# Performance work log

Hardware: AMD Instinct MI355X
Metric: run time of the kernel (lower is better)

Reference implementation:

```python
import jax, jax.numpy as jnp
import numpy as np


def _phi(z, conv_w, conv_b):
    # z: (H, W, S, 1) -> 3x3 SAME conv over state channels -> softmax over states
    x = jnp.transpose(z[..., 0], (2, 0, 1))[None]  # (1, S, H, W)
    y = jax.lax.conv_general_dilated(
        x, conv_w, window_strides=(1, 1), padding='SAME',
        dimension_numbers=('NCHW', 'OIHW', 'NCHW')) + conv_b[None, :, None, None]
    return jax.nn.softmax(jnp.transpose(y[0], (1, 2, 0)), axis=2)[..., None]  # (H, W, S, 1)


def _update(obs, P, u_k, w_k_O, conv_w, conv_b):
    H, W, O = obs.shape
    S = P.shape[0]
    # b = P^T @ obs per cell: b[h,w,s] = sum_o P[o,s] * obs[h,w,o]
    b = jnp.einsum('os,hwo->hws', P, obs)[..., None]  # (H, W, S, 1)
    # Analytic Jacobian db/dP: deriv_b[h,w,s,0,i,j] = obs[h,w,i] * delta(s==j)
    eye = jnp.eye(S, O, dtype=obs.dtype)
    deriv_b = (obs[:, :, None, :, None] * eye[None, None, :, None, :])[:, :, :, None, :, :]  # (H,W,S,1,S,O)

    Bu = b * u_k                                  # (H, W, S, 1)
    bu = jnp.sum(Bu, axis=2, keepdims=True)       # (H, W, 1, 1)
    Z = Bu / bu                                   # Bu / bu

    u_kp1 = _phi(Z, conv_w, conv_b)               # (H, W, S, 1)

    # Sensitivity recursion for obs params (quotient rule on Bu/bu)
    du = deriv_b * u_k[..., None, None] + b[..., None, None] * w_k_O  # (H,W,S,1,S,O)
    term1 = du * bu[..., None, None]
    term2 = jnp.expand_dims(jnp.sum(du, axis=2), 3) * Bu[..., None, None]
    w_pre = (term1 - term2) / bu[..., None, None] ** 2                # (H,W,S,1,S,O)

    # J @ w  ==  9 JVPs of Phi at Z with tangent columns of w (exact, avoids dense (HWS)^2 Jacobian)
    tangents = jnp.moveaxis(w_pre.reshape(H, W, S, 1, S * O), -1, 0)  # (S*O, H, W, S, 1)
    jvp1 = lambda t: jax.jvp(lambda z: _phi(z, conv_w, conv_b), (Z,), (t,))[1]
    w_kp1_O = jnp.moveaxis(jax.vmap(jvp1)(tangents), 0, -1).reshape(H, W, S, 1, S, O)
    return u_kp1, w_kp1_O


def setup_inputs() -> dict:
    key = jax.random.key(0)
    k1, k2, k3 = jax.random.split(key, 3)
    H = W = 512
    S = O = 3
    obs = jax.random.uniform(k1, (H, W, O), dtype=jnp.float32)
    obs_param_matrix = jnp.ones((S, O), jnp.float32) / O          # row-stochastic init
    u_k = jnp.ones((H, W, S, 1), jnp.float32) / S                 # uniform belief
    w_k_O = jnp.zeros((H, W, S, 1, S, O), jnp.float32)
    conv_w = jax.random.normal(k2, (S, S, 3, 3), jnp.float32) * 0.1
    conv_b = jax.random.normal(k3, (S,), jnp.float32) * 0.1
    return {'obs': obs, 'obs_param_matrix': obs_param_matrix, 'u_k': u_k,
            'w_k_O': w_k_O, 'conv_w': conv_w, 'conv_b': conv_b}


def reference(obs, obs_param_matrix, u_k, w_k_O, conv_w, conv_b):
    return _update(obs, obs_param_matrix, u_k, w_k_O, conv_w, conv_b)
```

## Files before the change

kernel.cpp:

```cpp
#include <hip/hip_runtime.h>

#define IMH 512
#define IMW 512
#define TW 16
#define TH 16
#define HW_ (TW + 2)
#define HH_ (TH + 2)
#define NHALO (HW_ * HH_)
#define ROW 31

__global__ __launch_bounds__(256, 4)
void hmm_fused(const float* __restrict__ obs,
               const float* __restrict__ P,
               const float* __restrict__ u_k,
               const float* __restrict__ w_k,
               const float* __restrict__ conv_w,
               const float* __restrict__ conv_b,
               float* __restrict__ out) {
    __shared__ float lds[NHALO * ROW];

    const int tid = threadIdx.x;
    const int w0 = blockIdx.x * TW;
    const int h0 = blockIdx.y * TH;

    float Pm[9];
#pragma unroll
    for (int i = 0; i < 9; ++i) Pm[i] = P[i];

    for (int p = tid; p < NHALO; p += 256) {
        const int hh = h0 + p / HW_ - 1;
        const int ww = w0 + p % HW_ - 1;
        float* row = &lds[p * ROW];
        if (hh < 0 || hh >= IMH || ww < 0 || ww >= IMW) {
#pragma unroll
            for (int c = 0; c < 30; ++c) row[c] = 0.0f;
            continue;
        }
        const int pix = hh * IMW + ww;
        const float ov[3] = {obs[pix * 3 + 0], obs[pix * 3 + 1], obs[pix * 3 + 2]};
        const float us[3] = {u_k[pix * 3 + 0], u_k[pix * 3 + 1], u_k[pix * 3 + 2]};

        float b[3], Bu[3], bu = 0.0f;
#pragma unroll
        for (int s = 0; s < 3; ++s) {
            b[s] = Pm[0 * 3 + s] * ov[0] + Pm[1 * 3 + s] * ov[1] + Pm[2 * 3 + s] * ov[2];
            Bu[s] = b[s] * us[s];
            bu += Bu[s];
        }
        const float inv_bu = 1.0f / bu;
        float Z[3];
#pragma unroll
        for (int s = 0; s < 3; ++s) { Z[s] = Bu[s] * inv_bu; row[s] = Z[s]; }

        const float* wkp = &w_k[(size_t)pix * 27];
#pragma unroll
        for (int i = 0; i < 3; ++i) {
#pragma unroll
            for (int j = 0; j < 3; ++j) {
                const int ij = i * 3 + j;
                float du[3], sdu = 0.0f;
#pragma unroll
                for (int s = 0; s < 3; ++s) {
                    float d = b[s] * wkp[s * 9 + ij];
                    if (s == j) d += ov[i] * us[s];
                    du[s] = d;
                    sdu += d;
                }
#pragma unroll
                for (int s = 0; s < 3; ++s)
                    row[(1 + ij) * 3 + s] = (du[s] - sdu * Z[s]) * inv_bu;
            }
        }
    }

    float cw[81];
#pragma unroll
    for (int i = 0; i < 81; ++i) cw[i] = conv_w[i];
    const float cb[3] = {conv_b[0], conv_b[1], conv_b[2]};

    __syncthreads();

    const int tx = tid % TW, ty = tid / TW;
    const int hp = (ty + 1) * HW_ + (tx + 1);
    const int pix = (h0 + ty) * IMW + (w0 + tx);

    float p0, p1, p2;
    {
        float y[3] = {cb[0], cb[1], cb[2]};
#pragma unroll
        for (int ky = 0; ky < 3; ++ky) {
#pragma unroll
            for (int kx = 0; kx < 3; ++kx) {
                const float* nb = &lds[(hp + (ky - 1) * HW_ + (kx - 1)) * ROW];
                const float v0 = nb[0], v1 = nb[1], v2 = nb[2];
#pragma unroll
                for (int s = 0; s < 3; ++s)
                    y[s] += cw[s * 27 + 0 * 9 + ky * 3 + kx] * v0 +
                            cw[s * 27 + 1 * 9 + ky * 3 + kx] * v1 +
                            cw[s * 27 + 2 * 9 + ky * 3 + kx] * v2;
            }
        }
        const float m = fmaxf(y[0], fmaxf(y[1], y[2]));
        const float e0 = __expf(y[0] - m), e1 = __expf(y[1] - m), e2 = __expf(y[2] - m);
        const float inv = 1.0f / (e0 + e1 + e2);
        p0 = e0 * inv; p1 = e1 * inv; p2 = e2 * inv;
        out[pix * 3 + 0] = p0; out[pix * 3 + 1] = p1; out[pix * 3 + 2] = p2;
    }

    float wout[27];
#pragma unroll
    for (int g = 1; g < 10; ++g) {
        float a[3] = {0.0f, 0.0f, 0.0f};
#pragma unroll
        for (int ky = 0; ky < 3; ++ky) {
#pragma unroll
            for (int kx = 0; kx < 3; ++kx) {
                const float* nb = &lds[(hp + (ky - 1) * HW_ + (kx - 1)) * ROW];
                const float v0 = nb[g * 3 + 0], v1 = nb[g * 3 + 1], v2 = nb[g * 3 + 2];
#pragma unroll
                for (int s = 0; s < 3; ++s)
                    a[s] += cw[s * 27 + 0 * 9 + ky * 3 + kx] * v0 +
                            cw[s * 27 + 1 * 9 + ky * 3 + kx] * v1 +
                            cw[s * 27 + 2 * 9 + ky * 3 + kx] * v2;
            }
        }
        const float dot = p0 * a[0] + p1 * a[1] + p2 * a[2];
        const int ij = g - 1;
        wout[0 * 9 + ij] = p0 * (a[0] - dot);
        wout[1 * 9 + ij] = p1 * (a[1] - dot);
        wout[2 * 9 + ij] = p2 * (a[2] - dot);
    }

    __syncthreads();

#pragma unroll
    for (int c = 0; c < 27; ++c) lds[tid * 27 + c] = wout[c];
    __syncthreads();

    float* outw = out + IMH * IMW * 3;
    for (int idx = tid; idx < TW * TH * 27; idx += 256) {
        const int r = idx / (TW * 27);
        const int rem = idx - r * (TW * 27);
        outw[(h0 + r) * (IMW * 27) + w0 * 27 + rem] = lds[idx];
    }
}

extern "C" void kernel_launch(void* const* d_in, const int* in_sizes, int n_in,
                              void* d_out, int out_size, void* d_ws, size_t ws_size,
                              hipStream_t stream) {
    const float* obs    = (const float*)d_in[0];
    const float* P      = (const float*)d_in[1];
    const float* u_k    = (const float*)d_in[2];
    const float* w_k    = (const float*)d_in[3];
    const float* conv_w = (const float*)d_in[4];
    const float* conv_b = (const float*)d_in[5];
    float* out = (float*)d_out;

    dim3 grid(IMW / TW, IMH / TH);
    hmm_fused<<<grid, 256, 0, stream>>>(obs, P, u_k, w_k, conv_w, conv_b, out);
}
```

Baseline: 117.6 us.

## Split tile into two 16x8 halves with register prefetch and row-sliding conv work split

Each block now covers two 16x8 sub-tiles. Global loads for both halos are issued up front with vectorized loads into registers, so the second half's fetch overlaps the first half's compute. The 9 JVP channel groups are spread across threads: one thread per pixel handles the primal softmax plus the last group, and the other groups run in a row-sliding register pipeline with direct global stores, replacing the LDS staging write-back. This trades higher register pressure and scattered 27-strided stores for better latency hiding and work distribution.

```diff
diff --git a/kernel.cpp b/kernel.cpp
--- a/kernel.cpp
+++ b/kernel.cpp
@@ -3,11 +3,164 @@
 #define IMH 512
 #define IMW 512
 #define TW 16
-#define TH 16
+#define TH 8
 #define HW_ (TW + 2)
 #define HH_ (TH + 2)
 #define NHALO (HW_ * HH_)
+#define NPIX (TW * TH)
 #define ROW 31
+
+typedef float f4 __attribute__((ext_vector_type(4)));
+typedef float f4a __attribute__((ext_vector_type(4), aligned(4)));
+typedef float f2a __attribute__((ext_vector_type(2), aligned(4)));
+
+
+#define LOADPX(HH, WW, WREG, OV, US, OK) {                                        \
+    (OK) = !((HH) < 0 || (HH) >= IMH || (WW) < 0 || (WW) >= IMW);                 \
+    if (OK) {                                                                     \
+        const int pix_ = (HH) * IMW + (WW);                                       \
+        const f2a o01_ = *(const f2a*)(obs + pix_ * 3);                           \
+        (OV)[0] = o01_.x; (OV)[1] = o01_.y; (OV)[2] = obs[pix_ * 3 + 2];          \
+        const f2a u01_ = *(const f2a*)(u_k + pix_ * 3);                           \
+        (US)[0] = u01_.x; (US)[1] = u01_.y; (US)[2] = u_k[pix_ * 3 + 2];          \
+        const float* wkp_ = &w_k[(size_t)pix_ * 27];                              \
+        const f4a* v4_ = (const f4a*)wkp_;                                        \
+        const f4a a0_ = v4_[0], a1_ = v4_[1], a2_ = v4_[2];                       \
+        const f4a a3_ = v4_[3], a4_ = v4_[4], a5_ = v4_[5];                       \
+        const f2a a6_ = *(const f2a*)(wkp_ + 24);                                 \
+        (WREG)[0]=a0_.x;  (WREG)[1]=a0_.y;  (WREG)[2]=a0_.z;  (WREG)[3]=a0_.w;    \
+        (WREG)[4]=a1_.x;  (WREG)[5]=a1_.y;  (WREG)[6]=a1_.z;  (WREG)[7]=a1_.w;    \
+        (WREG)[8]=a2_.x;  (WREG)[9]=a2_.y;  (WREG)[10]=a2_.z; (WREG)[11]=a2_.w;   \
+        (WREG)[12]=a3_.x; (WREG)[13]=a3_.y; (WREG)[14]=a3_.z; (WREG)[15]=a3_.w;   \
+        (WREG)[16]=a4_.x; (WREG)[17]=a4_.y; (WREG)[18]=a4_.z; (WREG)[19]=a4_.w;   \
+        (WREG)[20]=a5_.x; (WREG)[21]=a5_.y; (WREG)[22]=a5_.z; (WREG)[23]=a5_.w;   \
+        (WREG)[24]=a6_.x; (WREG)[25]=a6_.y; (WREG)[26]=wkp_[26];                  \
+    } }
+
+#define TRANSFORM(OK, WREG, OV, US, PIDX) {                                       \
+    float* row_ = &lds[(PIDX) * ROW];                                             \
+    if (!(OK)) {                                                                  \
+        _Pragma("unroll") for (int c = 0; c < 30; ++c) row_[c] = 0.0f;            \
+    } else {                                                                      \
+        float b_[3], Bu_[3], bu_ = 0.0f;                                          \
+        _Pragma("unroll")                                                         \
+        for (int s = 0; s < 3; ++s) {                                             \
+            b_[s] = Pm[0 + s] * (OV)[0] + Pm[3 + s] * (OV)[1] + Pm[6 + s] * (OV)[2]; \
+            Bu_[s] = b_[s] * (US)[s];                                             \
+            bu_ += Bu_[s];                                                        \
+        }                                                                         \
+        const float inv_bu_ = 1.0f / bu_;                                         \
+        float Z_[3];                                                              \
+        _Pragma("unroll")                                                         \
+        for (int s = 0; s < 3; ++s) { Z_[s] = Bu_[s] * inv_bu_; row_[s] = Z_[s]; }\
+        _Pragma("unroll")                                                         \
+        for (int i = 0; i < 3; ++i) {                                             \
+            _Pragma("unroll")                                                     \
+            for (int j = 0; j < 3; ++j) {                                         \
+                const int ij_ = i * 3 + j;                                        \
+                float du_[3], sdu_ = 0.0f;                                        \
+                _Pragma("unroll")                                                 \
+                for (int s = 0; s < 3; ++s) {                                     \
+                    float d_ = b_[s] * (WREG)[s * 9 + ij_];                       \
+                    if (s == j) d_ += (OV)[i] * (US)[s];                          \
+                    du_[s] = d_;                                                  \
+                    sdu_ += d_;                                                   \
+                }                                                                 \
+                _Pragma("unroll")                                                 \
+                for (int s = 0; s < 3; ++s)                                       \
+                    row_[(1 + ij_) * 3 + s] = (du_[s] - sdu_ * Z_[s]) * inv_bu_;  \
+            }                                                                     \
+        }                                                                         \
+    } }
+
+#define B0_BODY(H0T)                                                              \
+    if (tid < NPIX) {                                                             \
+        const int tx = tid & 15, ty = tid >> 4;                                   \
+        const int hp = (ty + 1) * HW_ + (tx + 1);                                 \
+        const int pix = ((H0T) + ty) * IMW + (w0 + tx);                           \
+        float y0 = cb0, y1 = cb1, y2 = cb2;                                       \
+        _Pragma("unroll")                                                         \
+        for (int ky = 0; ky < 3; ++ky) {                                          \
+            _Pragma("unroll")                                                     \
+            for (int kx = 0; kx < 3; ++kx) {                                      \
+                const float* nb = &lds[(hp + (ky - 1) * HW_ + (kx - 1)) * ROW];   \
+                const float v0 = nb[0], v1 = nb[1], v2 = nb[2];                   \
+                const int T = ky * 3 + kx;                                        \
+                y0 += cw[0 + T] * v0 + cw[9 + T] * v1 + cw[18 + T] * v2;          \
+                y1 += cw[27 + T] * v0 + cw[36 + T] * v1 + cw[45 + T] * v2;        \
+                y2 += cw[54 + T] * v0 + cw[63 + T] * v1 + cw[72 + T] * v2;        \
+            }                                                                     \
+        }                                                                         \
+        const float m_ = fmaxf(y0, fmaxf(y1, y2));                                \
+        const float e0 = __expf(y0 - m_), e1 = __expf(y1 - m_), e2 = __expf(y2 - m_); \
+        const float inv_ = 1.0f / (e0 + e1 + e2);                                 \
+        const float p0 = e0 * inv_, p1 = e1 * inv_, p2 = e2 * inv_;               \
+        out[pix * 3 + 0] = p0; out[pix * 3 + 1] = p1; out[pix * 3 + 2] = p2;      \
+        p_aux4[tid] = (f4){p0, p1, p2, 0.0f};                                     \
+        float a0 = 0.0f, a1 = 0.0f, a2 = 0.0f;                                    \
+        _Pragma("unroll")                                                         \
+        for (int ky = 0; ky < 3; ++ky) {                                          \
+            _Pragma("unroll")                                                     \
+            for (int kx = 0; kx < 3; ++kx) {                                      \
+                const float* nb = &lds[(hp + (ky - 1) * HW_ + (kx - 1)) * ROW];   \
+                const float v0 = nb[27], v1 = nb[28], v2 = nb[29];                \
+                const int T = ky * 3 + kx;                                        \
+                a0 += cw[0 + T] * v0 + cw[9 + T] * v1 + cw[18 + T] * v2;          \
+                a1 += cw[27 + T] * v0 + cw[36 + T] * v1 + cw[45 + T] * v2;        \
+                a2 += cw[54 + T] * v0 + cw[63 + T] * v1 + cw[72 + T] * v2;        \
+            }                                                                     \
+        }                                                                         \
+        const float dot_ = p0 * a0 + p1 * a1 + p2 * a2;                           \
+        float* wp = outw + (size_t)pix * 27;                                      \
+        wp[8]  = p0 * (a0 - dot_);                                                \
+        wp[17] = p1 * (a1 - dot_);                                                \
+        wp[26] = p2 * (a2 - dot_);                                                \
+    }
+
+#define ROWFMA(P0_, P1_, P2_, KY)                                                 \
+    P0_ += cw[0 + (KY)*3 + 0] * v00 + cw[9 + (KY)*3 + 0] * v01 + cw[18 + (KY)*3 + 0] * v02; \
+    P1_ += cw[27 + (KY)*3 + 0] * v00 + cw[36 + (KY)*3 + 0] * v01 + cw[45 + (KY)*3 + 0] * v02; \
+    P2_ += cw[54 + (KY)*3 + 0] * v00 + cw[63 + (KY)*3 + 0] * v01 + cw[72 + (KY)*3 + 0] * v02; \
+    P0_ += cw[0 + (KY)*3 + 1] * v10 + cw[9 + (KY)*3 + 1] * v11 + cw[18 + (KY)*3 + 1] * v12; \
+    P1_ += cw[27 + (KY)*3 + 1] * v10 + cw[36 + (KY)*3 + 1] * v11 + cw[45 + (KY)*3 + 1] * v12; \
+    P2_ += cw[54 + (KY)*3 + 1] * v10 + cw[63 + (KY)*3 + 1] * v11 + cw[72 + (KY)*3 + 1] * v12; \
+    P0_ += cw[0 + (KY)*3 + 2] * v20 + cw[9 + (KY)*3 + 2] * v21 + cw[18 + (KY)*3 + 2] * v22; \
+    P1_ += cw[27 + (KY)*3 + 2] * v20 + cw[36 + (KY)*3 + 2] * v21 + cw[45 + (KY)*3 + 2] * v22; \
+    P2_ += cw[54 + (KY)*3 + 2] * v20 + cw[63 + (KY)*3 + 2] * v21 + cw[72 + (KY)*3 + 2] * v22;
+
+#define FINISH(O, Q0, Q1, Q2) {                                                   \
+    const f4 pv = p_aux4[(O) * 16 + x];                                           \
+    const float dotf_ = pv.x * (Q0) + pv.y * (Q1) + pv.z * (Q2);                  \
+    float* wp_ = outw + ((size_t)((h0t + (O)) * IMW + (w0 + x))) * 27 + ij;       \
+    wp_[0]  = pv.x * ((Q0) - dotf_);                                              \
+    wp_[9]  = pv.y * ((Q1) - dotf_);                                              \
+    wp_[18] = pv.z * ((Q2) - dotf_); }
+
+#define STEP(R, N0,N1,N2, M0,M1,M2, O0,O1,O2, DO_N, DO_M, DO_O) {                 \
+    const int rb = ((rowb + (R)) * HW_ + x) * ROW + gch;                          \
+    const float v00 = lds[rb + 0],  v01 = lds[rb + 1],  v02 = lds[rb + 2];        \
+    const float v10 = lds[rb + 31], v11 = lds[rb + 32], v12 = lds[rb + 33];       \
+    const float v20 = lds[rb + 62], v21 = lds[rb + 63], v22 = lds[rb + 64];       \
+    if (DO_N) { N0 = 0.0f; N1 = 0.0f; N2 = 0.0f; ROWFMA(N0, N1, N2, 0) }          \
+    if (DO_M) { ROWFMA(M0, M1, M2, 1) }                                           \
+    if (DO_O) { ROWFMA(O0, O1, O2, 2) FINISH(rowb + (R) - 2, O0, O1, O2) } }
+
+#define B1_BODY(H0T) {                                                            \
+    const int h0t = (H0T);                                                        \
+    const int x = tid & 15;                                                       \
+    const int g = ((tid >> 4) & 7) + 1;                                           \
+    const int ij = g - 1;                                                         \
+    const int gch = 3 * g;                                                        \
+    const int hlf = tid >> 7;                                                     \
+    const int rowb = hlf * 4;                                                     \
+    float a00, a01, a02, b10, b11, b12, c20, c21, c22;                            \
+    STEP(0, a00,a01,a02, b10,b11,b12, c20,c21,c22, true,  false, false)           \
+    STEP(1, b10,b11,b12, a00,a01,a02, c20,c21,c22, true,  true,  false)           \
+    STEP(2, c20,c21,c22, b10,b11,b12, a00,a01,a02, true,  true,  true )           \
+    STEP(3, a00,a01,a02, c20,c21,c22, b10,b11,b12, true,  true,  true )           \
+    STEP(4, b10,b11,b12, a00,a01,a02, c20,c21,c22, false, true,  true )           \
+    STEP(5, c20,c21,c22, b10,b11,b12, a00,a01,a02, false, false, true )           \
+    }
 
 __global__ __launch_bounds__(256, 4)
 void hmm_fused(const float* __restrict__ obs,
@@ -17,132 +170,48 @@
                const float* __restrict__ conv_w,
                const float* __restrict__ conv_b,
                float* __restrict__ out) {
-    __shared__ float lds[NHALO * ROW];
+    __shared__ __align__(16) float lds[NHALO * ROW];
+    __shared__ f4 p_aux4[NPIX];
 
     const int tid = threadIdx.x;
     const int w0 = blockIdx.x * TW;
-    const int h0 = blockIdx.y * TH;
+    const int h0a = blockIdx.y * (2 * TH);
+    const int h0b = h0a + TH;
 
     float Pm[9];
 #pragma unroll
     for (int i = 0; i < 9; ++i) Pm[i] = P[i];
-
-    for (int p = tid; p < NHALO; p += 256) {
-        const int hh = h0 + p / HW_ - 1;
-        const int ww = w0 + p % HW_ - 1;
-        float* row = &lds[p * ROW];
-        if (hh < 0 || hh >= IMH || ww < 0 || ww >= IMW) {
-#pragma unroll
-            for (int c = 0; c < 30; ++c) row[c] = 0.0f;
-            continue;
-        }
-        const int pix = hh * IMW + ww;
-        const float ov[3] = {obs[pix * 3 + 0], obs[pix * 3 + 1], obs[pix * 3 + 2]};
-        const float us[3] = {u_k[pix * 3 + 0], u_k[pix * 3 + 1], u_k[pix * 3 + 2]};
-
-        float b[3], Bu[3], bu = 0.0f;
-#pragma unroll
-        for (int s = 0; s < 3; ++s) {
-            b[s] = Pm[0 * 3 + s] * ov[0] + Pm[1 * 3 + s] * ov[1] + Pm[2 * 3 + s] * ov[2];
-            Bu[s] = b[s] * us[s];
-            bu += Bu[s];
-        }
-        const float inv_bu = 1.0f / bu;
-        float Z[3];
-#pragma unroll
-        for (int s = 0; s < 3; ++s) { Z[s] = Bu[s] * inv_bu; row[s] = Z[s]; }
-
-        const float* wkp = &w_k[(size_t)pix * 27];
-#pragma unroll
-        for (int i = 0; i < 3; ++i) {
-#pragma unroll
-            for (int j = 0; j < 3; ++j) {
-                const int ij = i * 3 + j;
-                float du[3], sdu = 0.0f;
-#pragma unroll
-                for (int s = 0; s < 3; ++s) {
-                    float d = b[s] * wkp[s * 9 + ij];
-                    if (s == j) d += ov[i] * us[s];
-                    du[s] = d;
-                    sdu += d;
-                }
-#pragma unroll
-                for (int s = 0; s < 3; ++s)
-                    row[(1 + ij) * 3 + s] = (du[s] - sdu * Z[s]) * inv_bu;
-            }
-        }
-    }
-
     float cw[81];
 #pragma unroll
     for (int i = 0; i < 81; ++i) cw[i] = conv_w[i];
-    const float cb[3] = {conv_b[0], conv_b[1], conv_b[2]};
-
-    __syncthreads();
-
-    const int tx = tid % TW, ty = tid / TW;
-    const int hp = (ty + 1) * HW_ + (tx + 1);
-    const int pix = (h0 + ty) * IMW + (w0 + tx);
-
-    float p0, p1, p2;
-    {
-        float y[3] = {cb[0], cb[1], cb[2]};
-#pragma unroll
-        for (int ky = 0; ky < 3; ++ky) {
-#pragma unroll
-            for (int kx = 0; kx < 3; ++kx) {
-                const float* nb = &lds[(hp + (ky - 1) * HW_ + (kx - 1)) * ROW];
-                const float v0 = nb[0], v1 = nb[1], v2 = nb[2];
-#pragma unroll
-                for (int s = 0; s < 3; ++s)
-                    y[s] += cw[s * 27 + 0 * 9 + ky * 3 + kx] * v0 +
-                            cw[s * 27 + 1 * 9 + ky * 3 + kx] * v1 +
-                            cw[s * 27 + 2 * 9 + ky * 3 + kx] * v2;
-            }
-        }
-        const float m = fmaxf(y[0], fmaxf(y[1], y[2]));
-        const float e0 = __expf(y[0] - m), e1 = __expf(y[1] - m), e2 = __expf(y[2] - m);
-        const float inv = 1.0f / (e0 + e1 + e2);
-        p0 = e0 * inv; p1 = e1 * inv; p2 = e2 * inv;
-        out[pix * 3 + 0] = p0; out[pix * 3 + 1] = p1; out[pix * 3 + 2] = p2;
+    const float cb0 = conv_b[0], cb1 = conv_b[1], cb2 = conv_b[2];
+
+    float* outw = out + IMH * IMW * 3;
+
+    float wreg1[27], ov1[3], us1[3];
+    bool ok1 = false;
+
+    if (tid < NHALO) {
+        const int ph = tid / HW_ - 1, pw = tid % HW_ - 1;
+        float wreg0[27], ov0[3], us0[3];
+        bool ok0;
+        LOADPX(h0a + ph, w0 + pw, wreg0, ov0, us0, ok0)
+        LOADPX(h0b + ph, w0 + pw, wreg1, ov1, us1, ok1)
+        TRANSFORM(ok0, wreg0, ov0, us0, tid)
     }
-
-    float wout[27];
-#pragma unroll
-    for (int g = 1; g < 10; ++g) {
-        float a[3] = {0.0f, 0.0f, 0.0f};
-#pragma unroll
-        for (int ky = 0; ky < 3; ++ky) {
-#pragma unroll
-            for (int kx = 0; kx < 3; ++kx) {
-                const float* nb = &lds[(hp + (ky - 1) * HW_ + (kx - 1)) * ROW];
-                const float v0 = nb[g * 3 + 0], v1 = nb[g * 3 + 1], v2 = nb[g * 3 + 2];
-#pragma unroll
-                for (int s = 0; s < 3; ++s)
-                    a[s] += cw[s * 27 + 0 * 9 + ky * 3 + kx] * v0 +
-                            cw[s * 27 + 1 * 9 + ky * 3 + kx] * v1 +
-                            cw[s * 27 + 2 * 9 + ky * 3 + kx] * v2;
-            }
-        }
-        const float dot = p0 * a[0] + p1 * a[1] + p2 * a[2];
-        const int ij = g - 1;
-        wout[0 * 9 + ij] = p0 * (a[0] - dot);
-        wout[1 * 9 + ij] = p1 * (a[1] - dot);
-        wout[2 * 9 + ij] = p2 * (a[2] - dot);
-    }
-
-    __syncthreads();
-
-#pragma unroll
-    for (int c = 0; c < 27; ++c) lds[tid * 27 + c] = wout[c];
-    __syncthreads();
-
-    float* outw = out + IMH * IMW * 3;
-    for (int idx = tid; idx < TW * TH * 27; idx += 256) {
-        const int r = idx / (TW * 27);
-        const int rem = idx - r * (TW * 27);
-        outw[(h0 + r) * (IMW * 27) + w0 * 27 + rem] = lds[idx];
-    }
+    __syncthreads();
+
+    B0_BODY(h0a)
+    __syncthreads();
+    B1_BODY(h0a)
+    __syncthreads();
+
+    if (tid < NHALO) { TRANSFORM(ok1, wreg1, ov1, us1, tid) }
+    __syncthreads();
+
+    B0_BODY(h0b)
+    __syncthreads();
+    B1_BODY(h0b)
 }
 
 extern "C" void kernel_launch(void* const* d_in, const int* in_sizes, int n_in,
@@ -156,6 +225,6 @@
     const float* conv_b = (const float*)d_in[5];
     float* out = (float*)d_out;
 
-    dim3 grid(IMW / TW, IMH / TH);
+    dim3 grid(IMW / TW, IMH / (2 * TH));
     hmm_fused<<<grid, 256, 0, stream>>>(obs, P, u_k, w_k, conv_w, conv_b, out);
 }
```

After: 136.8 us. 16.3% more time.
